# Kernel optimization log

Hardware: AMD Instinct MI355X
Metric: run time of the kernel (lower is better)

Reference implementation:

```python
import jax, jax.numpy as jnp
import numpy as np
import math

B, N_SEQ, SEQ_LEN, C_M = 1, 256, 256, 256
N_HEADS, C_HIDDEN = 8, 32
HC = N_HEADS * C_HIDDEN
LN_EPS = 1e-5


def setup_inputs() -> dict:
    key = jax.random.key(0)
    ks = jax.random.split(key, 8)
    s_in = 1.0 / math.sqrt(C_M)
    s_out = 1.0 / math.sqrt(HC)
    return {
        "m": jax.random.normal(ks[0], (B, N_SEQ, SEQ_LEN, C_M), dtype=jnp.float32),
        "ln_w": jnp.ones((C_M,), dtype=jnp.float32),
        "ln_b": jnp.zeros((C_M,), dtype=jnp.float32),
        "wq": jax.random.normal(ks[1], (C_M, HC), dtype=jnp.float32) * s_in,
        "wk": jax.random.normal(ks[2], (C_M, HC), dtype=jnp.float32) * s_in,
        "wv": jax.random.normal(ks[3], (C_M, HC), dtype=jnp.float32) * s_in,
        "wg": jax.random.normal(ks[4], (C_M, HC), dtype=jnp.float32) * s_in,
        "bg": jnp.zeros((HC,), dtype=jnp.float32),
        "wo": jax.random.normal(ks[5], (HC, C_M), dtype=jnp.float32) * s_out,
        "bo": jnp.zeros((C_M,), dtype=jnp.float32),
    }


def reference(m, ln_w, ln_b, wq, wk, wv, wg, bg, wo, bo):
    b, s, l, _ = m.shape  # [B, n_seq, seq_len, c_m]
    # LayerNorm over c_m
    mu = jnp.mean(m, axis=-1, keepdims=True)
    var = jnp.mean(jnp.square(m - mu), axis=-1, keepdims=True)
    mn = (m - mu) * jax.lax.rsqrt(var + LN_EPS) * ln_w + ln_b  # [B, S, L, c_m]
    mt = jnp.swapaxes(mn, 1, 2)  # [B, L, S, c_m] -- attend over n_seq per column
    # QKV projections (no bias), split heads: [B, L, H, S, ch]
    def proj(w):
        return jnp.transpose(
            (mt @ w).reshape(b, l, s, N_HEADS, C_HIDDEN), (0, 1, 3, 2, 4)
        )
    q, k, v = proj(wq), proj(wk), proj(wv)
    logits = jnp.einsum("blhsc,blhtc->blhst", q, k) / math.sqrt(C_HIDDEN)
    weights = jax.nn.softmax(logits, axis=-1)
    o = jnp.einsum("blhst,blhtc->blhsc", weights, v)  # [B, L, H, S, ch]
    # Faithful to source: permute(0,2,1,3,4) -> [B, H, L, S, ch], then raw reshape
    o = jnp.transpose(o, (0, 2, 1, 3, 4))
    o = o.reshape(b, s, l, HC)  # data-scrambling reshape, as in source
    # Sigmoid gating on layer-normed input (m.transpose(1,2).transpose(1,2) == mn)
    g = jax.nn.sigmoid(mn @ wg + bg)  # [B, S, L, HC]
    o = g * o
    return o @ wo + bo  # [B, S, L, c_m]
```

## Files before the change

kernel.cpp:

```cpp
#include <hip/hip_runtime.h>

typedef unsigned short u16;
typedef __attribute__((ext_vector_type(8))) short bf16x8;
typedef __attribute__((ext_vector_type(4))) float f32x4;

__device__ __forceinline__ u16 f2b(float f){
  __bf16 h = (__bf16)f;
  return __builtin_bit_cast(u16, h);
}

__device__ __forceinline__ void gload_lds16(const void* g, void* l){
  __builtin_amdgcn_global_load_lds(
      (const __attribute__((address_space(1))) unsigned int*)g,
      (__attribute__((address_space(3))) unsigned int*)l, 16, 0, 0);
}

__global__ __launch_bounds__(256) void k_pre(const float* __restrict__ m,
    const float* __restrict__ lw, const float* __restrict__ lb,
    const float* __restrict__ wq, const float* __restrict__ wk,
    const float* __restrict__ wv, const float* __restrict__ wg,
    const float* __restrict__ wo,
    u16* __restrict__ mnb, u16* __restrict__ WT){
  __shared__ u16 T[16*264];
  int bx = blockIdx.x, tid = threadIdx.x;
  if (bx < 2048){
    int l = bx>>3;
    int w = tid>>6, ln = tid&63, half = ln>>5, lh = ln&31;
    float4 wa = *(const float4*)(lw + lh*8);
    float4 wb = *(const float4*)(lw + lh*8 + 4);
    float4 ba = *(const float4*)(lb + lh*8);
    float4 bb = *(const float4*)(lb + lh*8 + 4);
    #pragma unroll
    for (int i=0;i<4;++i){
      int s = (bx&7)*32 + w*8 + i*2 + half;
      const float* mp = m + ((size_t)s*256 + l)*256 + lh*8;
      float4 xa = *(const float4*)mp;
      float4 xb = *(const float4*)(mp+4);
      float s1 = (xa.x+xa.y)+(xa.z+xa.w) + (xb.x+xb.y)+(xb.z+xb.w);
      float s2 = xa.x*xa.x+xa.y*xa.y+xa.z*xa.z+xa.w*xa.w
               + xb.x*xb.x+xb.y*xb.y+xb.z*xb.z+xb.w*xb.w;
      #pragma unroll
      for (int off=16; off>0; off>>=1){
        s1 += __shfl_xor(s1, off);
        s2 += __shfl_xor(s2, off);
      }
      float mu  = s1*(1.0f/256.0f);
      float inv = rsqrtf(s2*(1.0f/256.0f) - mu*mu + 1e-5f);
      u16 o[8];
      o[0]=f2b((xa.x-mu)*inv*wa.x+ba.x);
      o[1]=f2b((xa.y-mu)*inv*wa.y+ba.y);
      o[2]=f2b((xa.z-mu)*inv*wa.z+ba.z);
      o[3]=f2b((xa.w-mu)*inv*wa.w+ba.w);
      o[4]=f2b((xb.x-mu)*inv*wb.x+bb.x);
      o[5]=f2b((xb.y-mu)*inv*wb.y+bb.y);
      o[6]=f2b((xb.z-mu)*inv*wb.z+bb.z);
      o[7]=f2b((xb.w-mu)*inv*wb.w+bb.w);
      u16* op = mnb + ((size_t)l*256 + s)*256 + lh*8;
      *(ushort4*)op     = *(ushort4*)&o[0];
      *(ushort4*)(op+4) = *(ushort4*)&o[4];
    }
  } else {
    int bb = bx - 2048;
    int z = bb>>4, n0 = (bb&15)*16;
    const float* W = (z==0)?wq:(z==1)?wk:(z==2)?wv:(z==3)?wg:wo;
    int nl = tid&15;
    #pragma unroll
    for (int i=0;i<16;++i){
      int cm = i*16 + (tid>>4);
      T[nl*264 + cm] = f2b(W[(size_t)cm*256 + n0 + nl]);
    }
    __syncthreads();
    int n = tid>>4, cc = (tid&15)*16;
    uint4 a = *(const uint4*)&T[n*264 + cc];
    uint4 c = *(const uint4*)&T[n*264 + cc + 8];
    *(uint4*)&WT[(size_t)z*65536 + (size_t)(n0+n)*256 + cc]     = a;
    *(uint4*)&WT[(size_t)z*65536 + (size_t)(n0+n)*256 + cc + 8] = c;
  }
}

__global__ __launch_bounds__(256,3) void k_fused(const u16* __restrict__ mnb,
    const u16* __restrict__ WT, const float* __restrict__ bg,
    const float* __restrict__ bo, float* __restrict__ outp){
  __shared__ u16 smem[27136];
  u16* KS  = smem + 2560;
  u16* VT2 = smem + 10752;
  u16* GAB = smem + 18944;
  float* OS = (float*)smem;
  u16* GS  = smem + 16384;

  int bx = blockIdx.x;
  int l = ((bx&7)<<5) | (bx>>6);
  int h = (bx>>3)&7;
  int tid = threadIdx.x;
  int lane = tid&63, wid = tid>>6, quad = lane>>4, lo = lane&15;
  int m0 = wid*64;
  u16* SC = smem + wid*640;
  f32x4 z4 = {0.f,0.f,0.f,0.f};
  int sp  = h*32 + (l>>3);
  int l0p = (l&7)*32;

  {
    const char* mb = (const char*)mnb;
    #pragma unroll
    for (int c2=0;c2<4;++c2){
      int r   = wid*8 + c2*2 + (lane>>5);
      int dst = (wid*8 + c2*2)*256;
      size_t src = (size_t)(l0p + r)*131072 + (size_t)sp*512
                 + (size_t)((((lane&31)*16) ^ ((r&7)<<4)));
      gload_lds16(mb + src, &GAB[dst]);
    }
  }

  const u16* Abase = mnb + (size_t)l*65536;
  const u16* Bq = WT + (size_t)h*32*256;
  const u16* Bk = WT + (size_t)65536 + (size_t)h*32*256;
  const u16* Bv = WT + (size_t)2*65536 + (size_t)h*32*256;
  f32x4 acc[4][6];
  #pragma unroll
  for (int a=0;a<4;++a)
    #pragma unroll
    for (int b=0;b<6;++b) acc[a][b]=z4;

  for (int ks=0; ks<8; ++ks){
    bf16x8 af[4];
    #pragma unroll
    for (int mt=0; mt<4; ++mt)
      af[mt] = *(const bf16x8*)(Abase + (size_t)(m0+mt*16+lo)*256 + ks*32 + quad*8);
    bf16x8 bq[2], bk2[2], bv2[2];
    #pragma unroll
    for (int c2=0; c2<2; ++c2){
      bq[c2]  = *(const bf16x8*)(Bq + (size_t)(c2*16+lo)*256 + ks*32 + quad*8);
      bk2[c2] = *(const bf16x8*)(Bk + (size_t)(c2*16+lo)*256 + ks*32 + quad*8);
      bv2[c2] = *(const bf16x8*)(Bv + (size_t)(c2*16+lo)*256 + ks*32 + quad*8);
    }
    #pragma unroll
    for (int mt=0; mt<4; ++mt){
      #pragma unroll
      for (int c2=0; c2<2; ++c2){
        acc[mt][0+c2] = __builtin_amdgcn_mfma_f32_16x16x32_bf16(af[mt], bq[c2],  acc[mt][0+c2], 0,0,0);
        acc[mt][2+c2] = __builtin_amdgcn_mfma_f32_16x16x32_bf16(af[mt], bk2[c2], acc[mt][2+c2], 0,0,0);
        acc[mt][4+c2] = __builtin_amdgcn_mfma_f32_16x16x32_bf16(af[mt], bv2[c2], acc[mt][4+c2], 0,0,0);
      }
    }
  }
  #pragma unroll
  for (int mt=0; mt<4; ++mt)
    #pragma unroll
    for (int ntl=0; ntl<2; ++ntl)
      #pragma unroll
      for (int r=0; r<4; ++r){
        int t = m0 + mt*16 + quad*4 + r;
        int c = ntl*16 + lo;
        KS[t*32 + c] = f2b(acc[mt][2+ntl][r]);
        VT2[(t>>3)*256 + c*8 + (t&7)] = f2b(acc[mt][4+ntl][r]);
      }
  bf16x8 qf[4];
  #pragma unroll
  for (int mt=0; mt<4; ++mt){
    #pragma unroll
    for (int ntl=0; ntl<2; ++ntl)
      #pragma unroll
      for (int r=0; r<4; ++r)
        SC[(quad*4+r)*40 + ntl*16+lo] = f2b(acc[mt][0+ntl][r]);
    qf[mt] = *(const bf16x8*)&SC[lo*40 + quad*8];
  }
  __syncthreads();

  const float scale = 0.17677669529663687f;
  float lr[16];
  #pragma unroll
  for (int i=0;i<16;++i) lr[i]=0.f;
  f32x4 o_acc[4][2];
  #pragma unroll
  for (int a=0;a<4;++a){ o_acc[a][0]=z4; o_acc[a][1]=z4; }

  for (int ts=0; ts<8; ++ts){
    bf16x8 kf[2];
    #pragma unroll
    for (int ntl=0; ntl<2; ++ntl)
      kf[ntl] = *(const bf16x8*)&KS[(ts*32+ntl*16+lo)*32 + quad*8];
    bf16x8 vf[2];
    #pragma unroll
    for (int nc=0; nc<2; ++nc)
      vf[nc] = *(const bf16x8*)&VT2[(ts*4+quad)*256 + (nc*16+lo)*8];
    #pragma unroll
    for (int mt=0; mt<4; ++mt){
      f32x4 sa[2];
      sa[0] = __builtin_amdgcn_mfma_f32_16x16x32_bf16(qf[mt], kf[0], z4, 0,0,0);
      sa[1] = __builtin_amdgcn_mfma_f32_16x16x32_bf16(qf[mt], kf[1], z4, 0,0,0);
      #pragma unroll
      for (int ntl=0; ntl<2; ++ntl)
        #pragma unroll
        for (int r=0; r<4; ++r){
          float p = __expf(sa[ntl][r]*scale);
          lr[mt*4+r] += p;
          SC[(quad*4+r)*40 + ntl*16+lo] = f2b(p);
        }
      bf16x8 paf = *(const bf16x8*)&SC[lo*40 + quad*8];
      o_acc[mt][0] = __builtin_amdgcn_mfma_f32_16x16x32_bf16(paf, vf[0], o_acc[mt][0], 0,0,0);
      o_acc[mt][1] = __builtin_amdgcn_mfma_f32_16x16x32_bf16(paf, vf[1], o_acc[mt][1], 0,0,0);
    }
  }
  #pragma unroll
  for (int i=0;i<16;++i){
    float v = lr[i];
    v += __shfl_xor(v, 1);
    v += __shfl_xor(v, 2);
    v += __shfl_xor(v, 4);
    v += __shfl_xor(v, 8);
    lr[i] = 1.0f / v;
  }
  __syncthreads();
  #pragma unroll
  for (int mt=0; mt<4; ++mt)
    #pragma unroll
    for (int nc=0; nc<2; ++nc)
      #pragma unroll
      for (int r=0; r<4; ++r){
        int s = m0 + mt*16 + quad*4 + r;
        int c = nc*16 + lo;
        OS[s*32 + c] = o_acc[mt][nc][r] * lr[mt*4+r];
      }
  __syncthreads();

  int wn0 = wid*64;
  const u16* Gw = WT + (size_t)3*65536;
  f32x4 gacc[2][4];
  #pragma unroll
  for (int a=0;a<2;++a)
    #pragma unroll
    for (int b=0;b<4;++b) gacc[a][b]=z4;
  for (int ks=0; ks<8; ++ks){
    bf16x8 ga[2];
    #pragma unroll
    for (int mt2=0; mt2<2; ++mt2){
      int j = mt2*16 + lo;
      ga[mt2] = *(const bf16x8*)&GAB[j*256 + ((ks*32 + quad*8) ^ ((j&7)<<3))];
    }
    bf16x8 gb[4];
    #pragma unroll
    for (int nt=0; nt<4; ++nt)
      gb[nt] = *(const bf16x8*)(Gw + (size_t)(wn0+nt*16+lo)*256 + ks*32 + quad*8);
    #pragma unroll
    for (int mt2=0; mt2<2; ++mt2)
      #pragma unroll
      for (int nt=0; nt<4; ++nt)
        gacc[mt2][nt] = __builtin_amdgcn_mfma_f32_16x16x32_bf16(ga[mt2], gb[nt], gacc[mt2][nt], 0,0,0);
  }
  __syncthreads();
  #pragma unroll
  for (int nt=0; nt<4; ++nt){
    int n = wn0 + nt*16 + lo;
    float bgn = bg[n];
    #pragma unroll
    for (int mt2=0; mt2<2; ++mt2)
      #pragma unroll
      for (int r=0; r<4; ++r){
        int j = mt2*16 + quad*4 + r;
        float g = 1.f/(1.f + __expf(-(gacc[mt2][nt][r] + bgn)));
        GS[j*264 + n] = f2b(g * OS[j*256 + n]);
      }
  }
  __syncthreads();

  const u16* Ow = WT + (size_t)4*65536;
  f32x4 pacc[2][4];
  #pragma unroll
  for (int a=0;a<2;++a)
    #pragma unroll
    for (int b=0;b<4;++b) pacc[a][b]=z4;
  for (int ks=0; ks<8; ++ks){
    bf16x8 pa[2];
    #pragma unroll
    for (int mt2=0; mt2<2; ++mt2)
      pa[mt2] = *(const bf16x8*)&GS[(mt2*16+lo)*264 + ks*32 + quad*8];
    bf16x8 pb[4];
    #pragma unroll
    for (int nt=0; nt<4; ++nt)
      pb[nt] = *(const bf16x8*)(Ow + (size_t)(wn0+nt*16+lo)*256 + ks*32 + quad*8);
    #pragma unroll
    for (int mt2=0; mt2<2; ++mt2)
      #pragma unroll
      for (int nt=0; nt<4; ++nt)
        pacc[mt2][nt] = __builtin_amdgcn_mfma_f32_16x16x32_bf16(pa[mt2], pb[nt], pacc[mt2][nt], 0,0,0);
  }
  #pragma unroll
  for (int nt=0; nt<4; ++nt){
    int n = wn0 + nt*16 + lo;
    float bon = bo[n];
    #pragma unroll
    for (int mt2=0; mt2<2; ++mt2)
      #pragma unroll
      for (int r=0; r<4; ++r){
        int j = mt2*16 + quad*4 + r;
        outp[((size_t)sp*256 + l0p + j)*256 + n] = pacc[mt2][nt][r] + bon;
      }
  }
}

extern "C" void kernel_launch(void* const* d_in, const int* in_sizes, int n_in,
                              void* d_out, int out_size, void* d_ws, size_t ws_size,
                              hipStream_t stream){
  const float* m  = (const float*)d_in[0];
  const float* lw = (const float*)d_in[1];
  const float* lb = (const float*)d_in[2];
  const float* wq = (const float*)d_in[3];
  const float* wk = (const float*)d_in[4];
  const float* wv = (const float*)d_in[5];
  const float* wg = (const float*)d_in[6];
  const float* bg = (const float*)d_in[7];
  const float* wo = (const float*)d_in[8];
  const float* bo = (const float*)d_in[9];

  u16* mnb = (u16*)d_ws;
  u16* WT  = mnb + (size_t)16777216;
  float* out = (float*)d_out;

  k_pre  <<<2128, 256, 0, stream>>>(m, lw, lb, wq, wk, wv, wg, wo, mnb, WT);
  k_fused<<<2048, 256, 0, stream>>>(mnb, WT, bg, bo, out);
}
```

Baseline: 300.4 us.

## Rework LDS layout for Q/K/V and load gate inputs directly from global

Q is now staged in a shared QS buffer, V is stored transposed with padded rows, and each wave keeps a full 64-row P buffer instead of a small per-tile scratch. The async global-to-LDS prefetch of the gate-projection A tile is removed; that operand is now read straight from global memory inside the gate GEMM loop. This lowers the LDS footprint and drops one barrier. The cost is that the gate GEMM reads come from global/L2 on the critical path with no prefetch to overlap them.

```diff
diff --git a/kernel.cpp b/kernel.cpp
--- a/kernel.cpp
+++ b/kernel.cpp
@@ -7,12 +7,6 @@
 __device__ __forceinline__ u16 f2b(float f){
   __bf16 h = (__bf16)f;
   return __builtin_bit_cast(u16, h);
-}
-
-__device__ __forceinline__ void gload_lds16(const void* g, void* l){
-  __builtin_amdgcn_global_load_lds(
-      (const __attribute__((address_space(1))) unsigned int*)g,
-      (__attribute__((address_space(3))) unsigned int*)l, 16, 0, 0);
 }
 
 __global__ __launch_bounds__(256) void k_pre(const float* __restrict__ m,
@@ -81,12 +75,13 @@
 __global__ __launch_bounds__(256,3) void k_fused(const u16* __restrict__ mnb,
     const u16* __restrict__ WT, const float* __restrict__ bg,
     const float* __restrict__ bo, float* __restrict__ outp){
-  __shared__ u16 smem[27136];
-  u16* KS  = smem + 2560;
-  u16* VT2 = smem + 10752;
-  u16* GAB = smem + 18944;
+  __shared__ u16 smem[26880];
+  u16* QS = smem;
+  u16* KS = smem + 10240;
+  u16* VT = smem + 18432;
+  u16* PB = smem;
   float* OS = (float*)smem;
-  u16* GS  = smem + 16384;
+  u16* GS = smem + 18432;
 
   int bx = blockIdx.x;
   int l = ((bx&7)<<5) | (bx>>6);
@@ -94,22 +89,7 @@
   int tid = threadIdx.x;
   int lane = tid&63, wid = tid>>6, quad = lane>>4, lo = lane&15;
   int m0 = wid*64;
-  u16* SC = smem + wid*640;
   f32x4 z4 = {0.f,0.f,0.f,0.f};
-  int sp  = h*32 + (l>>3);
-  int l0p = (l&7)*32;
-
-  {
-    const char* mb = (const char*)mnb;
-    #pragma unroll
-    for (int c2=0;c2<4;++c2){
-      int r   = wid*8 + c2*2 + (lane>>5);
-      int dst = (wid*8 + c2*2)*256;
-      size_t src = (size_t)(l0p + r)*131072 + (size_t)sp*512
-                 + (size_t)((((lane&31)*16) ^ ((r&7)<<4)));
-      gload_lds16(mb + src, &GAB[dst]);
-    }
-  }
 
   const u16* Abase = mnb + (size_t)l*65536;
   const u16* Bq = WT + (size_t)h*32*256;
@@ -149,21 +129,15 @@
     for (int ntl=0; ntl<2; ++ntl)
       #pragma unroll
       for (int r=0; r<4; ++r){
-        int t = m0 + mt*16 + quad*4 + r;
-        int c = ntl*16 + lo;
-        KS[t*32 + c] = f2b(acc[mt][2+ntl][r]);
-        VT2[(t>>3)*256 + c*8 + (t&7)] = f2b(acc[mt][4+ntl][r]);
+        int s = m0 + mt*16 + quad*4 + r;
+        QS[s*40 + ntl*16+lo] = f2b(acc[mt][0+ntl][r]);
+        KS[s*32 + ntl*16+lo] = f2b(acc[mt][2+ntl][r]);
+        VT[(ntl*16+lo)*264 + s] = f2b(acc[mt][4+ntl][r]);
       }
   bf16x8 qf[4];
   #pragma unroll
-  for (int mt=0; mt<4; ++mt){
-    #pragma unroll
-    for (int ntl=0; ntl<2; ++ntl)
-      #pragma unroll
-      for (int r=0; r<4; ++r)
-        SC[(quad*4+r)*40 + ntl*16+lo] = f2b(acc[mt][0+ntl][r]);
-    qf[mt] = *(const bf16x8*)&SC[lo*40 + quad*8];
-  }
+  for (int mt=0; mt<4; ++mt)
+    qf[mt] = *(const bf16x8*)&QS[(m0+mt*16+lo)*40 + quad*8];
   __syncthreads();
 
   const float scale = 0.17677669529663687f;
@@ -173,6 +147,7 @@
   f32x4 o_acc[4][2];
   #pragma unroll
   for (int a=0;a<4;++a){ o_acc[a][0]=z4; o_acc[a][1]=z4; }
+  int pbase = wid*64*40;
 
   for (int ts=0; ts<8; ++ts){
     bf16x8 kf[2];
@@ -182,7 +157,7 @@
     bf16x8 vf[2];
     #pragma unroll
     for (int nc=0; nc<2; ++nc)
-      vf[nc] = *(const bf16x8*)&VT2[(ts*4+quad)*256 + (nc*16+lo)*8];
+      vf[nc] = *(const bf16x8*)&VT[(nc*16+lo)*264 + ts*32 + quad*8];
     #pragma unroll
     for (int mt=0; mt<4; ++mt){
       f32x4 sa[2];
@@ -194,9 +169,9 @@
         for (int r=0; r<4; ++r){
           float p = __expf(sa[ntl][r]*scale);
           lr[mt*4+r] += p;
-          SC[(quad*4+r)*40 + ntl*16+lo] = f2b(p);
+          PB[pbase + (mt*16+quad*4+r)*40 + ntl*16+lo] = f2b(p);
         }
-      bf16x8 paf = *(const bf16x8*)&SC[lo*40 + quad*8];
+      bf16x8 paf = *(const bf16x8*)&PB[pbase + (mt*16+lo)*40 + quad*8];
       o_acc[mt][0] = __builtin_amdgcn_mfma_f32_16x16x32_bf16(paf, vf[0], o_acc[mt][0], 0,0,0);
       o_acc[mt][1] = __builtin_amdgcn_mfma_f32_16x16x32_bf16(paf, vf[1], o_acc[mt][1], 0,0,0);
     }
@@ -223,6 +198,8 @@
       }
   __syncthreads();
 
+  int sp  = h*32 + (l>>3);
+  int l0p = (l&7)*32;
   int wn0 = wid*64;
   const u16* Gw = WT + (size_t)3*65536;
   f32x4 gacc[2][4];
@@ -233,10 +210,8 @@
   for (int ks=0; ks<8; ++ks){
     bf16x8 ga[2];
     #pragma unroll
-    for (int mt2=0; mt2<2; ++mt2){
-      int j = mt2*16 + lo;
-      ga[mt2] = *(const bf16x8*)&GAB[j*256 + ((ks*32 + quad*8) ^ ((j&7)<<3))];
-    }
+    for (int mt2=0; mt2<2; ++mt2)
+      ga[mt2] = *(const bf16x8*)(mnb + ((size_t)(l0p+mt2*16+lo)*256 + sp)*256 + ks*32 + quad*8);
     bf16x8 gb[4];
     #pragma unroll
     for (int nt=0; nt<4; ++nt)
@@ -247,7 +222,6 @@
       for (int nt=0; nt<4; ++nt)
         gacc[mt2][nt] = __builtin_amdgcn_mfma_f32_16x16x32_bf16(ga[mt2], gb[nt], gacc[mt2][nt], 0,0,0);
   }
-  __syncthreads();
   #pragma unroll
   for (int nt=0; nt<4; ++nt){
     int n = wn0 + nt*16 + lo;
```

New measurement: 301.5 us. No clear change (+0.4%).
